# Optimization experiments

Measured on AMD Instinct MI355X. Metric: run time of the kernel, lower is better.

## Reference

```python
import jax, jax.numpy as jnp
import numpy as np

MEM_DIM = 4096
FEATURE_DIM = 1024
BATCH = 16384
EPS = 1e-12


def setup_inputs() -> dict:
    key = jax.random.key(0)
    k_z, k_mem = jax.random.split(key)
    z = jax.random.normal(k_z, (BATCH, FEATURE_DIM), dtype=jnp.float32)
    # torch reset_parameters: uniform(-stdv, stdv) with stdv = 1/sqrt(feature_dim)
    stdv = 1.0 / np.sqrt(FEATURE_DIM)
    memory = jax.random.uniform(k_mem, (MEM_DIM, FEATURE_DIM), dtype=jnp.float32,
                                minval=-stdv, maxval=stdv)
    return {"z": z, "memory": memory}


def hard_shrink_relu(w, lambd, eps=EPS):
    # relu(w - lambd) * w / (|w - lambd| + eps)
    d = w - lambd
    return jax.nn.relu(d) * w / (jnp.abs(d) + eps)


def reference(z, memory):
    # w: [B, M] attention scores over memory slots
    w = jnp.matmul(z, memory.T)
    w = jax.nn.softmax(w, axis=1)
    lambd = 2.0 / w.shape[1]  # default lambd = 2/N with N = mem_dim
    w_hat = hard_shrink_relu(w, lambd)
    att = jax.nn.softmax(w_hat, axis=1)
    z_hat = jnp.matmul(att, memory)  # [B, C]
    return (att, z_hat)
```

## Files before the change

### kernel.cpp

```cpp
#include <hip/hip_runtime.h>
#include <stdint.h>

#define BATCH   16384
#define MEM_DIM 4096
#define FEAT    1024
#define LAMBD   0.00048828125f
#define SEPS    1e-12f

typedef __attribute__((ext_vector_type(8))) short short8;
typedef __attribute__((ext_vector_type(4))) float f32x4;

__device__ __forceinline__ unsigned short f2bf(float x) {
  uint32_t u = __builtin_bit_cast(uint32_t, x);
  u += 0x7fffu + ((u >> 16) & 1u);
  return (unsigned short)(u >> 16);
}
__device__ __forceinline__ float bf2f(unsigned short b) {
  uint32_t u = ((uint32_t)b) << 16;
  return __builtin_bit_cast(float, u);
}

__global__ __launch_bounds__(256) void cast_bf16_kernel(
    const float* __restrict__ in, unsigned short* __restrict__ out) {
  size_t i = ((size_t)blockIdx.x * blockDim.x + threadIdx.x) * 8;
  float4 a = *(const float4*)(in + i);
  float4 b = *(const float4*)(in + i + 4);
  union { unsigned short u[8]; short8 v; } r;
  r.u[0] = f2bf(a.x); r.u[1] = f2bf(a.y); r.u[2] = f2bf(a.z); r.u[3] = f2bf(a.w);
  r.u[4] = f2bf(b.x); r.u[5] = f2bf(b.y); r.u[6] = f2bf(b.z); r.u[7] = f2bf(b.w);
  *(short8*)(out + i) = r.v;
}

__global__ __launch_bounds__(256) void transpose_cast_kernel(
    const float* __restrict__ in, unsigned short* __restrict__ out) {
  __shared__ unsigned short tile[32][33];
  const int mt = blockIdx.x;
  const int ct = blockIdx.y;
  const int tx = threadIdx.x & 31;
  const int ty = threadIdx.x >> 5;
  #pragma unroll
  for (int r = ty; r < 32; r += 8)
    tile[r][tx] = f2bf(in[(size_t)(mt * 32 + r) * FEAT + ct * 32 + tx]);
  __syncthreads();
  #pragma unroll
  for (int r = ty; r < 32; r += 8)
    out[(size_t)(ct * 32 + r) * MEM_DIM + mt * 32 + tx] = tile[tx][r];
}


#define LDSB(db, ab, h) ((((db)*2 + (ab))*2 + (h)) * 16384)

#define CFENCE asm volatile("" ::: "memory")
#define BAR()  do { CFENCE; __builtin_amdgcn_s_barrier(); CFENCE; } while (0)
#define LGKM0  asm volatile("s_waitcnt lgkmcnt(0)" ::: "memory")
#define VM4    asm volatile("s_waitcnt vmcnt(4)" ::: "memory")

#define STAGE(src, base, h, db, ab, kb) do {                                        \
    __builtin_amdgcn_global_load_lds(                                               \
      (const __attribute__((address_space(1))) uint32_t*)((src) + (base) +          \
          (size_t)(h) * 128 * K + rel0 + (kb)),                                     \
      (__attribute__((address_space(3))) uint32_t*)(lds + LDSB(db, ab, h) + tid*16),\
      16, 0, 0);                                                                    \
    __builtin_amdgcn_global_load_lds(                                               \
      (const __attribute__((address_space(1))) uint32_t*)((src) + (base) +          \
          (size_t)(h) * 128 * K + rel1 + (kb)),                                     \
      (__attribute__((address_space(3))) uint32_t*)(lds + LDSB(db, ab, h) + 8192 +  \
          tid*16),                                                                  \
      16, 0, 0);                                                                    \
  } while (0)

#define RD_A(db, mh)                                                                \
  _Pragma("unroll") for (int mi = 0; mi < 4; ++mi) {                                \
    _Pragma("unroll") for (int kk = 0; kk < 2; ++kk)                                \
      af[mi][kk] = *(const short8*)(aP##db + ((mh) << 13) + (mi << 11) + (kk << 10)); \
  }

#define RD_B2(db, n0)                                                               \
  _Pragma("unroll") for (int ni = 0; ni < 2; ++ni) {                                \
    _Pragma("unroll") for (int kk = 0; kk < 2; ++kk)                                \
      bfr[(n0) + ni][kk] = *(const short8*)(bP##db + (((n0) + ni) << 11) + (kk << 10)); \
  }

#define MFMA_Q(mh, nh) do {                                                         \
    __builtin_amdgcn_s_setprio(1);                                                  \
    _Pragma("unroll") for (int mi = 0; mi < 4; ++mi)                                \
    _Pragma("unroll") for (int ni = 0; ni < 2; ++ni)                                \
    _Pragma("unroll") for (int kk = 0; kk < 2; ++kk)                                \
      acc[(mh)*4 + mi][(nh)*2 + ni] = __builtin_amdgcn_mfma_f32_16x16x32_bf16(      \
          af[mi][kk], bfr[(nh)*2 + ni][kk], acc[(mh)*4 + mi][(nh)*2 + ni], 0, 0, 0);\
    __builtin_amdgcn_s_setprio(0);                                                  \
  } while (0)

template<bool OUT_BF16>
__global__ __launch_bounds__(512, 2)
void gemm256(const unsigned short* __restrict__ A, const unsigned short* __restrict__ Bt,
             float* __restrict__ Cf, unsigned short* __restrict__ Cb,
             const int K, const int ldc, const int nbn)
{
  __shared__ __align__(16) char lds[131072];

  const int tid  = threadIdx.x;
  const int lane = tid & 63;
  const int wid  = tid >> 6;
  const int wm = wid >> 2;
  const int wn = wid & 3;
  const int lrow = lane & 15;
  const int lkg  = lane >> 4;

  const int nwg = (int)gridDim.x;
  int wg = (int)blockIdx.x;
  wg = (wg & 7) * (nwg >> 3) + (wg >> 3);
  const int bm = wg / nbn;
  const int bn = wg % nbn;

  size_t rel0, rel1;
  {
    #pragma unroll
    for (int j = 0; j < 2; ++j) {
      const int c = j * 512 + tid;
      const int d = c * 16;
      const int s = d >> 10;
      int w = d & 1023;
      w ^= ((w >> 9) & 1) << 5;
      const int row  = ((s >> 1) << 4) + (w >> 6);
      const int colE = ((s & 1) << 5) + ((w & 63) >> 1);
      const size_t r = (size_t)row * K + colE;
      if (j == 0) rel0 = r; else rel1 = r;
    }
  }
  const size_t baseA = (size_t)bm * 256 * K;
  const size_t baseB = (size_t)bn * 256 * K;

  const int lane_base = (((lrow << 6) | (lkg << 4)) ^ ((((lrow >> 3) & 1)) << 5));
  const char* aP0 = lds + LDSB(0, 0, 0) + wm * 16384 + lane_base;
  const char* aP1 = lds + LDSB(1, 0, 0) + wm * 16384 + lane_base;
  const char* bP0 = lds + LDSB(0, 1, 0) + (wn >> 1) * 16384 + ((wn & 1) << 13) + lane_base;
  const char* bP1 = lds + LDSB(1, 1, 0) + (wn >> 1) * 16384 + ((wn & 1) << 13) + lane_base;

  f32x4 acc[8][4] = {};
  short8 af[4][2], bfr[4][2];

  const int NT  = K >> 6;
  const int NIT = K >> 7;

  STAGE(A,  baseA, 0, 0, 0, 0);
  STAGE(A,  baseA, 1, 0, 0, 0);
  STAGE(Bt, baseB, 0, 0, 1, 0);
  STAGE(Bt, baseB, 1, 0, 1, 0);
  STAGE(Bt, baseB, 0, 1, 1, 64);
  STAGE(Bt, baseB, 1, 1, 1, 64);
  VM4;
  BAR();

  for (int it = 0; it < NIT; ++it) {
    const int t2 = 2 * it + 2, t3 = 2 * it + 3;
    const int kb1 = (2 * it + 1) * 64;
    const int kb2 = (t2 < NT) ? t2 * 64 : 0;
    const int kb3 = (t3 < NT) ? t3 * 64 : 0;

    RD_A(0, 0); RD_B2(0, 0);
    STAGE(A, baseA, 0, 1, 0, kb1);
    BAR(); LGKM0; MFMA_Q(0, 0); BAR();
    RD_B2(0, 2);
    STAGE(A, baseA, 1, 1, 0, kb1);
    BAR(); LGKM0; MFMA_Q(0, 1); BAR();
    RD_A(0, 1);
    STAGE(Bt, baseB, 0, 0, 1, kb2);
    BAR(); LGKM0; MFMA_Q(1, 0); BAR();
    STAGE(Bt, baseB, 1, 0, 1, kb2);
    BAR(); LGKM0; MFMA_Q(1, 1); VM4; BAR();

    RD_A(1, 0); RD_B2(1, 0);
    STAGE(A, baseA, 0, 0, 0, kb2);
    BAR(); LGKM0; MFMA_Q(0, 0); BAR();
    RD_B2(1, 2);
    STAGE(A, baseA, 1, 0, 0, kb2);
    BAR(); LGKM0; MFMA_Q(0, 1); BAR();
    RD_A(1, 1);
    STAGE(Bt, baseB, 0, 1, 1, kb3);
    BAR(); LGKM0; MFMA_Q(1, 0); BAR();
    STAGE(Bt, baseB, 1, 1, 1, kb3);
    BAR(); LGKM0; MFMA_Q(1, 1); VM4; BAR();
  }

  const int row0 = bm * 256 + wm * 128 + lkg * 4;
  const int col0 = bn * 256 + wn * 64 + lrow;
  #pragma unroll
  for (int mi = 0; mi < 8; ++mi)
    #pragma unroll
    for (int ni = 0; ni < 4; ++ni)
      #pragma unroll
      for (int r = 0; r < 4; ++r) {
        const size_t row = row0 + mi * 16 + r;
        const int col = col0 + ni * 16;
        if (OUT_BF16) Cb[row * ldc + col] = f2bf(acc[mi][ni][r]);
        else          Cf[row * ldc + col] = acc[mi][ni][r];
      }
}

__device__ __forceinline__ float block_reduce_max(float v, float* sred) {
  #pragma unroll
  for (int o = 32; o > 0; o >>= 1) v = fmaxf(v, __shfl_xor(v, o, 64));
  __syncthreads();
  if ((threadIdx.x & 63) == 0) sred[threadIdx.x >> 6] = v;
  __syncthreads();
  return fmaxf(fmaxf(sred[0], sred[1]), fmaxf(sred[2], sred[3]));
}
__device__ __forceinline__ float block_reduce_sum(float v, float* sred) {
  #pragma unroll
  for (int o = 32; o > 0; o >>= 1) v += __shfl_xor(v, o, 64);
  __syncthreads();
  if ((threadIdx.x & 63) == 0) sred[threadIdx.x >> 6] = v;
  __syncthreads();
  return (sred[0] + sred[1]) + (sred[2] + sred[3]);
}

__global__ __launch_bounds__(256)
void softmax_shrink_kernel(const unsigned short* __restrict__ W,
                           float* __restrict__ att,
                           unsigned short* __restrict__ attb)
{
  __shared__ float sred[4];
  const int row = blockIdx.x;
  const int tid = threadIdx.x;
  const unsigned short* wrp = W + (size_t)row * MEM_DIM + tid * 16;

  union { short8 v; unsigned short u[8]; } l0, l1;
  l0.v = *(const short8*)wrp;
  l1.v = *(const short8*)(wrp + 8);
  float v[16];
  #pragma unroll
  for (int j = 0; j < 8; ++j) { v[j] = bf2f(l0.u[j]); v[8 + j] = bf2f(l1.u[j]); }

  float m = v[0];
  #pragma unroll
  for (int j = 1; j < 16; ++j) m = fmaxf(m, v[j]);
  m = block_reduce_max(m, sred);
  float s = 0.f, e[16];
  #pragma unroll
  for (int j = 0; j < 16; ++j) { e[j] = __expf(v[j] - m); s += e[j]; }
  const float inv1 = 1.f / block_reduce_sum(s, sred);

  float wh[16];
  #pragma unroll
  for (int j = 0; j < 16; ++j) {
    const float p = e[j] * inv1;
    const float d = p - LAMBD;
    wh[j] = (d > 0.f) ? (d * p / (d + SEPS)) : 0.f;
  }

  float m2 = wh[0];
  #pragma unroll
  for (int j = 1; j < 16; ++j) m2 = fmaxf(m2, wh[j]);
  m2 = block_reduce_max(m2, sred);
  float s2 = 0.f, a[16];
  #pragma unroll
  for (int j = 0; j < 16; ++j) { a[j] = __expf(wh[j] - m2); s2 += a[j]; }
  const float inv2 = 1.f / block_reduce_sum(s2, sred);

  float* arow = att + (size_t)row * MEM_DIM + tid * 16;
  #pragma unroll
  for (int j = 0; j < 16; j += 4) {
    float4 o; o.x = a[j] * inv2; o.y = a[j+1] * inv2; o.z = a[j+2] * inv2; o.w = a[j+3] * inv2;
    *(float4*)(arow + j) = o;
  }
  union { short8 v; unsigned short u[8]; } s0, s1;
  #pragma unroll
  for (int j = 0; j < 8; ++j) { s0.u[j] = f2bf(a[j] * inv2); s1.u[j] = f2bf(a[8 + j] * inv2); }
  unsigned short* ab = attb + (size_t)row * MEM_DIM + tid * 16;
  *(short8*)ab = s0.v;
  *(short8*)(ab + 8) = s1.v;
}

extern "C" void kernel_launch(void* const* d_in, const int* in_sizes, int n_in,
                              void* d_out, int out_size, void* d_ws, size_t ws_size,
                              hipStream_t stream) {
  const float* z   = (const float*)d_in[0];
  const float* mem = (const float*)d_in[1];
  float* att_out  = (float*)d_out;
  float* zhat_out = (float*)d_out + (size_t)BATCH * MEM_DIM;

  unsigned short* zb    = (unsigned short*)d_ws;
  unsigned short* memb  = zb + (size_t)BATCH * FEAT;
  unsigned short* membT = memb + (size_t)MEM_DIM * FEAT;
  unsigned short* wbuf  = membT + (size_t)FEAT * MEM_DIM;

  cast_bf16_kernel<<<(BATCH * FEAT / 8) / 256, 256, 0, stream>>>(z, zb);
  cast_bf16_kernel<<<(MEM_DIM * FEAT / 8) / 256, 256, 0, stream>>>(mem, memb);
  transpose_cast_kernel<<<dim3(MEM_DIM / 32, FEAT / 32), 256, 0, stream>>>(mem, membT);

  gemm256<true><<<(MEM_DIM / 256) * (BATCH / 256), 512, 0, stream>>>(
      zb, memb, nullptr, wbuf, FEAT, MEM_DIM, MEM_DIM / 256);

  softmax_shrink_kernel<<<BATCH, 256, 0, stream>>>(wbuf, att_out, wbuf);

  gemm256<false><<<(FEAT / 256) * (BATCH / 256), 512, 0, stream>>>(
      wbuf, membT, zhat_out, nullptr, MEM_DIM, FEAT, FEAT / 256);
}
```

Baseline: 394.4 us.

## Chain M-tiles per workgroup in first GEMM, fuse prep casts, use nontemporal IO

Merges the three cast and transpose kernels into one prep kernel, so memory is read once to produce both the bf16 copy and its transpose. The first GEMM becomes persistent-style: 256 workgroups each walk four consecutive M tiles with the same B tile, streaming the pipeline across tile boundaries and writing each tile's output mid-loop. Nontemporal loads and stores are added for the fp32 inputs and outputs. Routing M chunks to XCDs is meant to improve L2 reuse of B and cut launch and prologue overhead, but output stores now interrupt the pipelined loop.

```diff
diff --git a/kernel.cpp b/kernel.cpp
--- a/kernel.cpp
+++ b/kernel.cpp
@@ -20,31 +20,38 @@
   return __builtin_bit_cast(float, u);
 }
 
-__global__ __launch_bounds__(256) void cast_bf16_kernel(
-    const float* __restrict__ in, unsigned short* __restrict__ out) {
-  size_t i = ((size_t)blockIdx.x * blockDim.x + threadIdx.x) * 8;
-  float4 a = *(const float4*)(in + i);
-  float4 b = *(const float4*)(in + i + 4);
-  union { unsigned short u[8]; short8 v; } r;
-  r.u[0] = f2bf(a.x); r.u[1] = f2bf(a.y); r.u[2] = f2bf(a.z); r.u[3] = f2bf(a.w);
-  r.u[4] = f2bf(b.x); r.u[5] = f2bf(b.y); r.u[6] = f2bf(b.z); r.u[7] = f2bf(b.w);
-  *(short8*)(out + i) = r.v;
-}
-
-__global__ __launch_bounds__(256) void transpose_cast_kernel(
-    const float* __restrict__ in, unsigned short* __restrict__ out) {
-  __shared__ unsigned short tile[32][33];
-  const int mt = blockIdx.x;
-  const int ct = blockIdx.y;
-  const int tx = threadIdx.x & 31;
-  const int ty = threadIdx.x >> 5;
-  #pragma unroll
-  for (int r = ty; r < 32; r += 8)
-    tile[r][tx] = f2bf(in[(size_t)(mt * 32 + r) * FEAT + ct * 32 + tx]);
-  __syncthreads();
-  #pragma unroll
-  for (int r = ty; r < 32; r += 8)
-    out[(size_t)(ct * 32 + r) * MEM_DIM + mt * 32 + tx] = tile[tx][r];
+__global__ __launch_bounds__(256) void prep_kernel(
+    const float* __restrict__ z, const float* __restrict__ mem,
+    unsigned short* __restrict__ zb, unsigned short* __restrict__ memb,
+    unsigned short* __restrict__ membT) {
+  const int b = blockIdx.x;
+  if (b < 8192) {
+    size_t i = ((size_t)b * 256 + threadIdx.x) * 8;
+    f32x4 a = __builtin_nontemporal_load((const f32x4*)(z + i));
+    f32x4 c = __builtin_nontemporal_load((const f32x4*)(z + i + 4));
+    union { unsigned short u[8]; short8 v; } r;
+    r.u[0] = f2bf(a.x); r.u[1] = f2bf(a.y); r.u[2] = f2bf(a.z); r.u[3] = f2bf(a.w);
+    r.u[4] = f2bf(c.x); r.u[5] = f2bf(c.y); r.u[6] = f2bf(c.z); r.u[7] = f2bf(c.w);
+    *(short8*)(zb + i) = r.v;
+  } else {
+    __shared__ unsigned short tile[32][33];
+    const int bb = b - 8192;
+    const int mt = bb & 127;
+    const int ct = bb >> 7;
+    const int tx = threadIdx.x & 31;
+    const int ty = threadIdx.x >> 5;
+    #pragma unroll
+    for (int r = ty; r < 32; r += 8) {
+      const unsigned short bf =
+          f2bf(__builtin_nontemporal_load(mem + (size_t)(mt * 32 + r) * FEAT + ct * 32 + tx));
+      tile[r][tx] = bf;
+      memb[(size_t)(mt * 32 + r) * FEAT + ct * 32 + tx] = bf;
+    }
+    __syncthreads();
+    #pragma unroll
+    for (int r = ty; r < 32; r += 8)
+      membT[(size_t)(ct * 32 + r) * MEM_DIM + mt * 32 + tx] = tile[tx][r];
+  }
 }
 
 
@@ -58,12 +65,12 @@
 #define STAGE(src, base, h, db, ab, kb) do {                                        \
     __builtin_amdgcn_global_load_lds(                                               \
       (const __attribute__((address_space(1))) uint32_t*)((src) + (base) +          \
-          (size_t)(h) * 128 * K + rel0 + (kb)),                                     \
+          (size_t)(h) * 128 * KC + rel0 + (kb)),                                    \
       (__attribute__((address_space(3))) uint32_t*)(lds + LDSB(db, ab, h) + tid*16),\
       16, 0, 0);                                                                    \
     __builtin_amdgcn_global_load_lds(                                               \
       (const __attribute__((address_space(1))) uint32_t*)((src) + (base) +          \
-          (size_t)(h) * 128 * K + rel1 + (kb)),                                     \
+          (size_t)(h) * 128 * KC + rel1 + (kb)),                                    \
       (__attribute__((address_space(3))) uint32_t*)(lds + LDSB(db, ab, h) + 8192 +  \
           tid*16),                                                                  \
       16, 0, 0);                                                                    \
@@ -91,12 +98,15 @@
     __builtin_amdgcn_s_setprio(0);                                                  \
   } while (0)
 
-template<bool OUT_BF16>
+template<bool OUT_BF16, int KC, int CHAIN, int NBN>
 __global__ __launch_bounds__(512, 2)
 void gemm256(const unsigned short* __restrict__ A, const unsigned short* __restrict__ Bt,
-             float* __restrict__ Cf, unsigned short* __restrict__ Cb,
-             const int K, const int ldc, const int nbn)
+             float* __restrict__ Cf, unsigned short* __restrict__ Cb, const int ldc)
 {
+  constexpr int NT = KC / 64;
+  constexpr int LOG2NT = (NT == 16) ? 4 : 6;
+  constexpr int HNIT = NT / 2;
+
   __shared__ __align__(16) char lds[131072];
 
   const int tid  = threadIdx.x;
@@ -107,11 +117,22 @@
   const int lrow = lane & 15;
   const int lkg  = lane >> 4;
 
-  const int nwg = (int)gridDim.x;
-  int wg = (int)blockIdx.x;
-  wg = (wg & 7) * (nwg >> 3) + (wg >> 3);
-  const int bm = wg / nbn;
-  const int bn = wg % nbn;
+  int bm0, bn;
+  if constexpr (CHAIN == 4) {
+    const int bid = (int)blockIdx.x;
+    const int xcd = bid & 7;
+    const int t   = bid >> 3;
+    const int ghi = t >> 4;
+    bn = t & 15;
+    const int grp = ghi * 8 + xcd;
+    bm0 = grp * 4;
+  } else {
+    const int nwg = (int)gridDim.x;
+    int wg = (int)blockIdx.x;
+    wg = (wg & 7) * (nwg >> 3) + (wg >> 3);
+    bm0 = wg / NBN;
+    bn  = wg % NBN;
+  }
 
   size_t rel0, rel1;
   {
@@ -124,12 +145,20 @@
       w ^= ((w >> 9) & 1) << 5;
       const int row  = ((s >> 1) << 4) + (w >> 6);
       const int colE = ((s & 1) << 5) + ((w & 63) >> 1);
-      const size_t r = (size_t)row * K + colE;
+      const size_t r = (size_t)row * KC + colE;
       if (j == 0) rel0 = r; else rel1 = r;
     }
   }
-  const size_t baseA = (size_t)bm * 256 * K;
-  const size_t baseB = (size_t)bn * 256 * K;
+  const size_t baseA0 = (size_t)bm0 * 256 * KC;
+  const size_t segStep = (size_t)256 * KC;
+  const size_t baseB = (size_t)bn * 256 * KC;
+
+  auto baseAOf = [&](int g) {
+    int s = g >> LOG2NT;
+    if (s >= CHAIN) s = CHAIN - 1;
+    return baseA0 + (size_t)s * segStep;
+  };
+  auto kbOf = [&](int g) { return (g & (NT - 1)) * 64; };
 
   const int lane_base = (((lrow << 6) | (lkg << 4)) ^ ((((lrow >> 3) & 1)) << 5));
   const char* aP0 = lds + LDSB(0, 0, 0) + wm * 16384 + lane_base;
@@ -140,11 +169,8 @@
   f32x4 acc[8][4] = {};
   short8 af[4][2], bfr[4][2];
 
-  const int NT  = K >> 6;
-  const int NIT = K >> 7;
-
-  STAGE(A,  baseA, 0, 0, 0, 0);
-  STAGE(A,  baseA, 1, 0, 0, 0);
+  STAGE(A,  baseA0, 0, 0, 0, 0);
+  STAGE(A,  baseA0, 1, 0, 0, 0);
   STAGE(Bt, baseB, 0, 0, 1, 0);
   STAGE(Bt, baseB, 1, 0, 1, 0);
   STAGE(Bt, baseB, 0, 1, 1, 64);
@@ -152,17 +178,17 @@
   VM4;
   BAR();
 
-  for (int it = 0; it < NIT; ++it) {
-    const int t2 = 2 * it + 2, t3 = 2 * it + 3;
-    const int kb1 = (2 * it + 1) * 64;
-    const int kb2 = (t2 < NT) ? t2 * 64 : 0;
-    const int kb3 = (t3 < NT) ? t3 * 64 : 0;
+  #pragma unroll 1
+  for (int git = 0; git < CHAIN * HNIT; ++git) {
+    const int g1 = 2 * git + 1, g2 = 2 * git + 2, g3 = 2 * git + 3;
+    const size_t bA1 = baseAOf(g1), bA2 = baseAOf(g2);
+    const int kb1 = kbOf(g1), kb2 = kbOf(g2), kb3 = kbOf(g3);
 
     RD_A(0, 0); RD_B2(0, 0);
-    STAGE(A, baseA, 0, 1, 0, kb1);
+    STAGE(A, bA1, 0, 1, 0, kb1);
     BAR(); LGKM0; MFMA_Q(0, 0); BAR();
     RD_B2(0, 2);
-    STAGE(A, baseA, 1, 1, 0, kb1);
+    STAGE(A, bA1, 1, 1, 0, kb1);
     BAR(); LGKM0; MFMA_Q(0, 1); BAR();
     RD_A(0, 1);
     STAGE(Bt, baseB, 0, 0, 1, kb2);
@@ -171,31 +197,36 @@
     BAR(); LGKM0; MFMA_Q(1, 1); VM4; BAR();
 
     RD_A(1, 0); RD_B2(1, 0);
-    STAGE(A, baseA, 0, 0, 0, kb2);
+    STAGE(A, bA2, 0, 0, 0, kb2);
     BAR(); LGKM0; MFMA_Q(0, 0); BAR();
     RD_B2(1, 2);
-    STAGE(A, baseA, 1, 0, 0, kb2);
+    STAGE(A, bA2, 1, 0, 0, kb2);
     BAR(); LGKM0; MFMA_Q(0, 1); BAR();
     RD_A(1, 1);
     STAGE(Bt, baseB, 0, 1, 1, kb3);
     BAR(); LGKM0; MFMA_Q(1, 0); BAR();
     STAGE(Bt, baseB, 1, 1, 1, kb3);
     BAR(); LGKM0; MFMA_Q(1, 1); VM4; BAR();
-  }
-
-  const int row0 = bm * 256 + wm * 128 + lkg * 4;
-  const int col0 = bn * 256 + wn * 64 + lrow;
-  #pragma unroll
-  for (int mi = 0; mi < 8; ++mi)
-    #pragma unroll
-    for (int ni = 0; ni < 4; ++ni)
+
+    if (((git + 1) & (HNIT - 1)) == 0) {
+      const int s = ((git + 1) >> (LOG2NT - 1)) - 1;
+      const int row0 = (bm0 + s) * 256 + wm * 128 + lkg * 4;
+      const int col0 = bn * 256 + wn * 64 + lrow;
       #pragma unroll
-      for (int r = 0; r < 4; ++r) {
-        const size_t row = row0 + mi * 16 + r;
-        const int col = col0 + ni * 16;
-        if (OUT_BF16) Cb[row * ldc + col] = f2bf(acc[mi][ni][r]);
-        else          Cf[row * ldc + col] = acc[mi][ni][r];
-      }
+      for (int mi = 0; mi < 8; ++mi)
+        #pragma unroll
+        for (int ni = 0; ni < 4; ++ni) {
+          #pragma unroll
+          for (int r = 0; r < 4; ++r) {
+            const size_t row = row0 + mi * 16 + r;
+            const int col = col0 + ni * 16;
+            if (OUT_BF16) Cb[row * ldc + col] = f2bf(acc[mi][ni][r]);
+            else __builtin_nontemporal_store(acc[mi][ni][r], &Cf[row * ldc + col]);
+          }
+          acc[mi][ni] = (f32x4){0.f, 0.f, 0.f, 0.f};
+        }
+    }
+  }
 }
 
 __device__ __forceinline__ float block_reduce_max(float v, float* sred) {
@@ -261,8 +292,8 @@
   float* arow = att + (size_t)row * MEM_DIM + tid * 16;
   #pragma unroll
   for (int j = 0; j < 16; j += 4) {
-    float4 o; o.x = a[j] * inv2; o.y = a[j+1] * inv2; o.z = a[j+2] * inv2; o.w = a[j+3] * inv2;
-    *(float4*)(arow + j) = o;
+    f32x4 o = {a[j] * inv2, a[j+1] * inv2, a[j+2] * inv2, a[j+3] * inv2};
+    __builtin_nontemporal_store(o, (f32x4*)(arow + j));
   }
   union { short8 v; unsigned short u[8]; } s0, s1;
   #pragma unroll
@@ -285,15 +316,11 @@
   unsigned short* membT = memb + (size_t)MEM_DIM * FEAT;
   unsigned short* wbuf  = membT + (size_t)FEAT * MEM_DIM;
 
-  cast_bf16_kernel<<<(BATCH * FEAT / 8) / 256, 256, 0, stream>>>(z, zb);
-  cast_bf16_kernel<<<(MEM_DIM * FEAT / 8) / 256, 256, 0, stream>>>(mem, memb);
-  transpose_cast_kernel<<<dim3(MEM_DIM / 32, FEAT / 32), 256, 0, stream>>>(mem, membT);
-
-  gemm256<true><<<(MEM_DIM / 256) * (BATCH / 256), 512, 0, stream>>>(
-      zb, memb, nullptr, wbuf, FEAT, MEM_DIM, MEM_DIM / 256);
+  prep_kernel<<<8192 + 4096, 256, 0, stream>>>(z, mem, zb, memb, membT);
+
+  gemm256<true, FEAT, 4, 16><<<256, 512, 0, stream>>>(zb, memb, nullptr, wbuf, MEM_DIM);
 
   softmax_shrink_kernel<<<BATCH, 256, 0, stream>>>(wbuf, att_out, wbuf);
 
-  gemm256<false><<<(FEAT / 256) * (BATCH / 256), 512, 0, stream>>>(
-      wbuf, membT, zhat_out, nullptr, MEM_DIM, FEAT, FEAT / 256);
-}
+  gemm256<false, MEM_DIM, 1, 4><<<256, 512, 0, stream>>>(wbuf, membT, zhat_out, nullptr, FEAT);
+}
```

Result: slower. 476.6 us (+20.8%).
